# Kernel optimization log

Measured on AMD Instinct MI355X. Metric: run time of the kernel, lower is better.

Reference implementation:

```python
import jax, jax.numpy as jnp
import numpy as np

B, T, DIM = 4, 2048, 1024
H, DH = 16, 64  # num_heads, dim_head = dim // num_heads


def setup_inputs() -> dict:
    key = jax.random.key(0)
    k1, k2, k3 = jax.random.split(key, 3)
    x = jax.random.normal(k1, (B, T, DIM), dtype=jnp.float32)
    # nn.Linear weights stored as [out_features, in_features]
    w_qkv = jax.random.normal(k2, (3 * H * DH, DIM), dtype=jnp.float32) * (DIM ** -0.5)
    w_out = jax.random.normal(k3, (DIM, H * DH), dtype=jnp.float32) * ((H * DH) ** -0.5)
    b_out = jnp.zeros((DIM,), dtype=jnp.float32)
    return {"x": x, "w_qkv": w_qkv, "w_out": w_out, "b_out": b_out}


def reference(x, w_qkv, w_out, b_out):
    b, t, dim = x.shape
    # qkv projection (Linear, no bias): [b, t, 3*H*DH]
    qkv = jnp.einsum('btd,ed->bte', x, w_qkv)
    # einops 'b t (d k h) -> k b h t d' with k=3, h=H: dim_head outermost, heads innermost
    qkv = qkv.reshape(b, t, DH, 3, H)            # [b, t, d, k, h]
    qkv = jnp.transpose(qkv, (3, 0, 4, 1, 2))    # [k, b, h, t, d]
    q, k_, v = qkv[0], qkv[1], qkv[2]
    scale = dim ** -0.5  # note: scales by dim, not dim_head (faithful to source)
    attn = jnp.einsum('bhid,bhjd->bhij', q, k_) * scale
    attn = jax.nn.softmax(attn, axis=-1)
    out = jnp.einsum('bhij,bhjd->bhid', attn, v)  # [b, h, t, d]
    # 'b h t d -> b t (h d)'
    out = jnp.transpose(out, (0, 2, 1, 3)).reshape(b, t, H * DH)
    return jnp.einsum('bte,de->btd', out, w_out) + b_out
```

## Files before the change

### kernel.cpp

```cpp
#include <hip/hip_runtime.h>
#include <stdint.h>

typedef unsigned short ushort_t;
typedef __attribute__((ext_vector_type(8))) short short8;
typedef __attribute__((ext_vector_type(4))) short short4v;
typedef __attribute__((ext_vector_type(4))) float f32x4;
typedef __attribute__((ext_vector_type(16))) float f32x16;

#define B_ 4
#define T_ 2048
#define H_ 16
#define DH_ 64
#define DIM_ 1024
#define NE_ 3072
#define LOG2E 1.4426950408889634f

__device__ __forceinline__ ushort_t f2bf(float f) {
  union { float f; uint32_t u; } v; v.f = f;
  uint32_t u = v.u;
  uint32_t r = (u + 0x7FFFu + ((u >> 16) & 1u)) >> 16;
  return (ushort_t)r;
}
__device__ __forceinline__ void gload16(const void* g, void* l) {
  __builtin_amdgcn_global_load_lds(
      (__attribute__((address_space(1))) void*)g,
      (__attribute__((address_space(3))) void*)l, 16, 0, 0);
}
__device__ __forceinline__ uint32_t cvtpk(float a, float b) {
  uint32_t r;
  asm("v_cvt_pk_bf16_f32 %0, %1, %2" : "=v"(r) : "v"(a), "v"(b));
  return r;
}
__device__ __forceinline__ float exp2_asm(float x) {
  float r; asm("v_exp_f32 %0, %1" : "=v"(r) : "v"(x)); return r;
}

__global__ __launch_bounds__(256)
void cvt3(const float* __restrict__ a, ushort_t* __restrict__ oa, long nba,
          const float* __restrict__ b, ushort_t* __restrict__ ob, long nbb,
          const float* __restrict__ c, ushort_t* __restrict__ oc) {
  long i = ((long)blockIdx.x * 256 + threadIdx.x) * 4;
  const float* src; ushort_t* dst;
  if (i < nba)            { src = a; dst = oa; }
  else if (i < nba + nbb) { src = b; dst = ob; i -= nba; }
  else                    { src = c; dst = oc; i -= nba + nbb; }
  const float4 v = *(const float4*)(src + i);
  short4v o;
  o[0] = (short)f2bf(v.x); o[1] = (short)f2bf(v.y);
  o[2] = (short)f2bf(v.z); o[3] = (short)f2bf(v.w);
  *(short4v*)(dst + i) = o;
}

template<int MODE>
__global__ __launch_bounds__(256)
void gemm_bt(const ushort_t* __restrict__ A, const ushort_t* __restrict__ Bm,
             ushort_t* __restrict__ Cb, float* __restrict__ Cf,
             const float* __restrict__ bias, int M, int N, int K, int nb) {
  __shared__ __align__(16) ushort_t Alds[128 * 32];
  __shared__ __align__(16) ushort_t Blds[128 * 32];
  const int tid = threadIdx.x;
  const int wave = tid >> 6, lane = tid & 63;
  const int cpx = gridDim.x >> 3;
  const int bid = (blockIdx.x & 7) * cpx + (blockIdx.x >> 3);
  const int bm0 = (bid / nb) << 7, bn0 = (bid % nb) << 7;
  const int l4 = lane >> 4, l15 = lane & 15;
  const int srow = lane >> 2;
  const int scol = (lane & 3) * 8;
  const int wr = (wave >> 1) * 64, wc = (wave & 1) * 64;

  f32x4 acc[4][4];
#pragma unroll
  for (int i = 0; i < 4; ++i)
#pragma unroll
    for (int j = 0; j < 4; ++j) acc[i][j] = {0.f, 0.f, 0.f, 0.f};

  for (int k0 = 0; k0 < K; k0 += 32) {
    __syncthreads();
#pragma unroll
    for (int c = 0; c < 2; ++c) {
      const int r0 = wave * 32 + c * 16;
      gload16(A + (long)(bm0 + r0 + srow) * K + k0 + scol, Alds + r0 * 32);
      gload16(Bm + (long)(bn0 + r0 + srow) * K + k0 + scol, Blds + r0 * 32);
    }
    __syncthreads();
    short8 af[4], bfr[4];
#pragma unroll
    for (int i = 0; i < 4; ++i)
      af[i] = *(const short8*)(Alds + (wr + i * 16 + l15) * 32 + l4 * 8);
#pragma unroll
    for (int j = 0; j < 4; ++j)
      bfr[j] = *(const short8*)(Blds + (wc + j * 16 + l15) * 32 + l4 * 8);
#pragma unroll
    for (int i = 0; i < 4; ++i)
#pragma unroll
      for (int j = 0; j < 4; ++j)
        acc[i][j] = __builtin_amdgcn_mfma_f32_16x16x32_bf16(af[i], bfr[j], acc[i][j], 0, 0, 0);
  }

#pragma unroll
  for (int i = 0; i < 4; ++i) {
    const int row = bm0 + wr + i * 16 + l4 * 4;
#pragma unroll
    for (int j = 0; j < 4; ++j) {
      const int col = bn0 + wc + j * 16 + l15;
      if (MODE == 0) {
        const float mult = (((col >> 4) % 3) == 0) ? 0.04508422f : 1.f;
#pragma unroll
        for (int r = 0; r < 4; ++r)
          Cb[(long)(row + r) * N + col] = f2bf(acc[i][j][r] * mult);
      } else {
        const float add = bias[col];
#pragma unroll
        for (int r = 0; r < 4; ++r)
          Cf[(long)(row + r) * N + col] = acc[i][j][r] + add;
      }
    }
  }
}

__global__ __launch_bounds__(256)
void reorg(const ushort_t* __restrict__ qkv, ushort_t* __restrict__ Qh,
           ushort_t* __restrict__ Kh, ushort_t* __restrict__ Vth) {
  __shared__ __align__(16) ushort_t lds[8 * 3080];
  const int bid = blockIdx.x;
  const int tt = bid & 255, b = bid >> 8;
  const int t0 = tt * 8;
  const int tid = threadIdx.x;
  const short8* src = (const short8*)(qkv + ((long)(b * T_ + t0)) * NE_);
  short8* dst = (short8*)lds;
  for (int i = tid; i < 8 * 384; i += 256) {
    const int r = i / 384, c = i - r * 384;
    dst[r * 385 + c] = src[i];
  }
  __syncthreads();
  for (int i = tid; i < 16 * 8 * 8; i += 256) {
    const int dblk = i & 7, t = (i >> 3) & 7, h = i >> 6;
    short8 vq, vk;
#pragma unroll
    for (int e = 0; e < 8; ++e) {
      const int d = dblk * 8 + e;
      vq[e] = (short)lds[t * 3080 + d * 48 + h];
      vk[e] = (short)lds[t * 3080 + d * 48 + 16 + h];
    }
    const long o = ((long)((b * H_ + h) * T_) + t0 + t) * DH_ + dblk * 8;
    *(short8*)(Qh + o) = vq;
    *(short8*)(Kh + o) = vk;
  }
  for (int i = tid; i < 16 * 64; i += 256) {
    const int d = i & 63, h = i >> 6;
    short8 v0;
#pragma unroll
    for (int t = 0; t < 8; ++t) v0[t] = (short)lds[t * 3080 + d * 48 + 32 + h];
    const long o = ((long)((b * H_ + h) * DH_) + d) * T_ + t0;
    *(short8*)(Vth + o) = v0;
  }
}

#define MFMA32(a, b, c) __builtin_amdgcn_mfma_f32_32x32x16_bf16(a, b, c, 0, 0, 0)

__global__ __launch_bounds__(256, 4)
void attn_fwd6(const ushort_t* __restrict__ Qh, const ushort_t* __restrict__ Kh,
               const ushort_t* __restrict__ Vth, ushort_t* __restrict__ aout) {
  __shared__ __align__(16) ushort_t Kt[2][64 * 64];
  __shared__ __align__(16) ushort_t Vts[2][64 * 64];
  const int bid = blockIdx.x;
  const int xcd = bid & 7, idx = bid >> 3;
  const int bh = xcd + ((idx & 7) << 3);
  const int qb = idx >> 3;
  const int tid = threadIdx.x, wv = tid >> 6, lane = tid & 63;
  const int l31 = lane & 31, hi = lane >> 5, l7 = lane & 7, l8 = lane >> 3;
  const ushort_t* Qb = Qh + (long)bh * T_ * DH_;
  const ushort_t* Kb = Kh + (long)bh * T_ * DH_;
  const ushort_t* Vb = Vth + (long)bh * DH_ * T_;
  const int q = qb * 128 + wv * 32 + l31;

  short8 qf[4];
#pragma unroll
  for (int s = 0; s < 4; ++s)
    qf[s] = *(const short8*)(Qb + (long)q * DH_ + s * 16 + hi * 8);

  f32x16 acc0, acc1, z16;
#pragma unroll
  for (int i = 0; i < 16; ++i) { acc0[i] = 0.f; acc1[i] = 0.f; z16[i] = 0.f; }
  float lsum_part = 0.f;

  const int r0a = wv * 16;
  const int sl = ((l7 ^ l8) * 8);

#define STAGE(bufi, jj)                                                          \
  do {                                                                           \
    _Pragma("unroll")                                                            \
    for (int c = 0; c < 2; ++c) {                                                \
      const int rr = r0a + c * 8 + l8;                                           \
      gload16(Kb + (long)((jj) + rr) * DH_ + sl, &Kt[bufi][(r0a + c * 8) * 64]); \
      gload16(Vb + (long)rr * T_ + (jj) + sl, &Vts[bufi][(r0a + c * 8) * 64]);   \
    }                                                                            \
  } while (0)

  STAGE(0, 0);
  asm volatile("s_waitcnt vmcnt(0)" ::: "memory");
  __builtin_amdgcn_sched_barrier(0);
  __builtin_amdgcn_s_barrier();
  __builtin_amdgcn_sched_barrier(0);

  int buf = 0;
  for (int j0 = 0; j0 < T_; j0 += 64) {
    STAGE(buf ^ 1, (j0 + 64) & (T_ - 1));

    const ushort_t* Ktb = &Kt[buf][0];
    const ushort_t* Vtb = &Vts[buf][0];

    f32x16 sb0, sb1;
    __builtin_amdgcn_s_setprio(1);
#pragma unroll
    for (int s = 0; s < 4; ++s) {
      const int so = ((2 * s + hi) ^ l7) * 8;
      const short8 k0 = *(const short8*)(Ktb + (l31) * 64 + so);
      const short8 k1 = *(const short8*)(Ktb + (32 + l31) * 64 + so);
      sb0 = MFMA32(k0, qf[s], (s == 0) ? z16 : sb0);
      sb1 = MFMA32(k1, qf[s], (s == 0) ? z16 : sb1);
    }
    __builtin_amdgcn_s_setprio(0);

    float r0 = 0.f, r1 = 0.f, r2 = 0.f, r3 = 0.f;
#pragma unroll
    for (int i = 0; i < 16; i += 4) {
      sb0[i]     = exp2_asm(sb0[i]);     r0 += sb0[i];
      sb0[i + 1] = exp2_asm(sb0[i + 1]); r1 += sb0[i + 1];
      sb0[i + 2] = exp2_asm(sb0[i + 2]); r2 += sb0[i + 2];
      sb0[i + 3] = exp2_asm(sb0[i + 3]); r3 += sb0[i + 3];
    }
#pragma unroll
    for (int i = 0; i < 16; i += 4) {
      sb1[i]     = exp2_asm(sb1[i]);     r0 += sb1[i];
      sb1[i + 1] = exp2_asm(sb1[i + 1]); r1 += sb1[i + 1];
      sb1[i + 2] = exp2_asm(sb1[i + 2]); r2 += sb1[i + 2];
      sb1[i + 3] = exp2_asm(sb1[i + 3]); r3 += sb1[i + 3];
    }
    lsum_part += (r0 + r1) + (r2 + r3);

    short8 pf[4];
#pragma unroll
    for (int ks = 0; ks < 4; ++ks) {
      const f32x16& S = (ks < 2) ? sb0 : sb1;
      const int rb = (ks & 1) * 8;
      uint32_t wE0 = cvtpk(S[rb + 0], S[rb + 1]);
      uint32_t wE1 = cvtpk(S[rb + 2], S[rb + 3]);
      uint32_t wO0 = cvtpk(S[rb + 4], S[rb + 5]);
      uint32_t wO1 = cvtpk(S[rb + 6], S[rb + 7]);
      asm("v_permlane32_swap_b32 %0, %1" : "+v"(wE0), "+v"(wO0));
      asm("v_permlane32_swap_b32 %0, %1" : "+v"(wE1), "+v"(wO1));
      union { uint32_t u[4]; short8 v; } pk;
      pk.u[0] = wE0; pk.u[1] = wE1; pk.u[2] = wO0; pk.u[3] = wO1;
      pf[ks] = pk.v;
    }

    __builtin_amdgcn_s_setprio(1);
#pragma unroll
    for (int ks = 0; ks < 4; ++ks) {
      const int so = ((2 * ks + hi) ^ l7) * 8;
      const short8 v0 = *(const short8*)(Vtb + (l31) * 64 + so);
      const short8 v1 = *(const short8*)(Vtb + (32 + l31) * 64 + so);
      acc0 = MFMA32(v0, pf[ks], acc0);
      acc1 = MFMA32(v1, pf[ks], acc1);
    }
    __builtin_amdgcn_s_setprio(0);

    asm volatile("s_waitcnt vmcnt(0)" ::: "memory");
    __builtin_amdgcn_sched_barrier(0);
    __builtin_amdgcn_s_barrier();
    __builtin_amdgcn_sched_barrier(0);
    buf ^= 1;
  }

  const float lsum = lsum_part + __shfl_xor(lsum_part, 32);
  const float inv = 1.f / lsum;
  const int b = bh >> 4, h = bh & 15;
  ushort_t* orow = aout + ((long)(b * T_ + q)) * DIM_ + h * DH_;
#pragma unroll
  for (int vb = 0; vb < 2; ++vb)
#pragma unroll
    for (int rg = 0; rg < 4; ++rg) {
      short4v o4;
#pragma unroll
      for (int e = 0; e < 4; ++e) {
        const float val = ((vb == 0) ? acc0[rg * 4 + e] : acc1[rg * 4 + e]) * inv;
        o4[e] = (short)f2bf(val);
      }
      *(short4v*)(orow + vb * 32 + rg * 8 + hi * 4) = o4;
    }
}

extern "C" void kernel_launch(void* const* d_in, const int* in_sizes, int n_in,
                              void* d_out, int out_size, void* d_ws, size_t ws_size,
                              hipStream_t stream) {
  const float* x_f    = (const float*)d_in[0];
  const float* wqkv_f = (const float*)d_in[1];
  const float* wout_f = (const float*)d_in[2];
  const float* bout_f = (const float*)d_in[3];
  float* out = (float*)d_out;

  ushort_t* wqkv_bf = (ushort_t*)d_ws;
  ushort_t* wout_bf = wqkv_bf + (long)NE_ * DIM_;
  ushort_t* qkv     = wout_bf + (long)DIM_ * DIM_;
  ushort_t* R       = qkv + (long)B_ * T_ * NE_;
  ushort_t* x_bf = R;
  ushort_t* Qh   = R;
  ushort_t* Kh   = R + (long)B_ * H_ * T_ * DH_;
  ushort_t* Vth  = Kh + (long)B_ * H_ * T_ * DH_;
  ushort_t* aout = qkv;

  const long n_x = (long)B_ * T_ * DIM_;
  const long n_wq = (long)NE_ * DIM_;
  cvt3<<<dim3((int)((n_x + n_wq + (long)DIM_ * DIM_) / 1024)), dim3(256), 0, stream>>>(
      x_f, x_bf, n_x, wqkv_f, wqkv_bf, n_wq, wout_f, wout_bf);

  gemm_bt<0><<<dim3((8192 / 128) * (3072 / 128)), dim3(256), 0, stream>>>(
      x_bf, wqkv_bf, qkv, nullptr, nullptr, 8192, 3072, 1024, 3072 / 128);
  reorg<<<dim3(1024), dim3(256), 0, stream>>>(qkv, Qh, Kh, Vth);
  attn_fwd6<<<dim3(1024), dim3(256), 0, stream>>>(Qh, Kh, Vth, aout);
  gemm_bt<1><<<dim3((8192 / 128) * (1024 / 128)), dim3(256), 0, stream>>>(
      aout, wout_bf, nullptr, out, bout_f, 8192, 1024, 1024, 1024 / 128);
}
```

Before: 224.2 us.

## Replace GEMMs with 256x256 double-buffered, swizzled-LDS pipelined kernel

Both projection GEMMs now use 256x256 output tiles with 512 threads and a K-step of 64. LDS is double-buffered so the next tile's global loads are issued while MFMAs run on the current one. The LDS layout uses an XOR swizzle to avoid bank conflicts, and the wave schedule uses barrier phases and setprio. The aim is to raise operand reuse and hide load latency, but the grid shrinks a lot (384 and 128 blocks), which risks poor CU occupancy on the output projection.

```diff
diff --git a/kernel.cpp b/kernel.cpp
--- a/kernel.cpp
+++ b/kernel.cpp
@@ -51,71 +51,124 @@
   *(short4v*)(dst + i) = o;
 }
 
+#define MFMA16(a, b, c) __builtin_amdgcn_mfma_f32_16x16x32_bf16(a, b, c, 0, 0, 0)
+#define MFMA32(a, b, c) __builtin_amdgcn_mfma_f32_32x32x16_bf16(a, b, c, 0, 0, 0)
+
 template<int MODE>
-__global__ __launch_bounds__(256)
-void gemm_bt(const ushort_t* __restrict__ A, const ushort_t* __restrict__ Bm,
+__global__ __launch_bounds__(512, 2)
+void gemm256(const ushort_t* __restrict__ A, const ushort_t* __restrict__ Bm,
              ushort_t* __restrict__ Cb, float* __restrict__ Cf,
              const float* __restrict__ bias, int M, int N, int K, int nb) {
-  __shared__ __align__(16) ushort_t Alds[128 * 32];
-  __shared__ __align__(16) ushort_t Blds[128 * 32];
+  __shared__ __align__(16) ushort_t Al[2][256 * 64];
+  __shared__ __align__(16) ushort_t Bl[2][256 * 64];
   const int tid = threadIdx.x;
   const int wave = tid >> 6, lane = tid & 63;
   const int cpx = gridDim.x >> 3;
   const int bid = (blockIdx.x & 7) * cpx + (blockIdx.x >> 3);
-  const int bm0 = (bid / nb) << 7, bn0 = (bid % nb) << 7;
+  const int bm0 = (bid / nb) << 8, bn0 = (bid % nb) << 8;
   const int l4 = lane >> 4, l15 = lane & 15;
-  const int srow = lane >> 2;
-  const int scol = (lane & 3) * 8;
-  const int wr = (wave >> 1) * 64, wc = (wave & 1) * 64;
-
-  f32x4 acc[4][4];
-#pragma unroll
-  for (int i = 0; i < 4; ++i)
+  const int l7 = lane & 7, l8 = lane >> 3;
+  const int wm = wave >> 2, wn = wave & 3;
+  const int wrow0 = wm * 128, wcol0 = wn * 64;
+
+  const int sl = (l7 ^ l8) * 8;
+  const int r0a = wave * 32;
+
+#define GSTAGE(bufi, kk0)                                                          \
+  do {                                                                             \
+    _Pragma("unroll")                                                              \
+    for (int c = 0; c < 4; ++c) {                                                  \
+      const int rr = r0a + c * 8 + l8;                                             \
+      gload16(A + (long)(bm0 + rr) * K + (kk0) + sl, &Al[bufi][(r0a + c * 8) * 64]); \
+      gload16(Bm + (long)(bn0 + rr) * K + (kk0) + sl, &Bl[bufi][(r0a + c * 8) * 64]); \
+    }                                                                              \
+  } while (0)
+
+  f32x4 acc[8][4];
+#pragma unroll
+  for (int i = 0; i < 8; ++i)
 #pragma unroll
     for (int j = 0; j < 4; ++j) acc[i][j] = {0.f, 0.f, 0.f, 0.f};
 
-  for (int k0 = 0; k0 < K; k0 += 32) {
-    __syncthreads();
-#pragma unroll
-    for (int c = 0; c < 2; ++c) {
-      const int r0 = wave * 32 + c * 16;
-      gload16(A + (long)(bm0 + r0 + srow) * K + k0 + scol, Alds + r0 * 32);
-      gload16(Bm + (long)(bn0 + r0 + srow) * K + k0 + scol, Blds + r0 * 32);
-    }
-    __syncthreads();
-    short8 af[4], bfr[4];
-#pragma unroll
-    for (int i = 0; i < 4; ++i)
-      af[i] = *(const short8*)(Alds + (wr + i * 16 + l15) * 32 + l4 * 8);
-#pragma unroll
-    for (int j = 0; j < 4; ++j)
-      bfr[j] = *(const short8*)(Blds + (wc + j * 16 + l15) * 32 + l4 * 8);
-#pragma unroll
-    for (int i = 0; i < 4; ++i)
-#pragma unroll
-      for (int j = 0; j < 4; ++j)
-        acc[i][j] = __builtin_amdgcn_mfma_f32_16x16x32_bf16(af[i], bfr[j], acc[i][j], 0, 0, 0);
-  }
-
-#pragma unroll
-  for (int i = 0; i < 4; ++i) {
-    const int row = bm0 + wr + i * 16 + l4 * 4;
-#pragma unroll
-    for (int j = 0; j < 4; ++j) {
-      const int col = bn0 + wc + j * 16 + l15;
+  GSTAGE(0, 0);
+  asm volatile("s_waitcnt vmcnt(0)" ::: "memory");
+  __builtin_amdgcn_sched_barrier(0);
+  __builtin_amdgcn_s_barrier();
+  __builtin_amdgcn_sched_barrier(0);
+
+  const int NT = K >> 6;
+  int buf = 0;
+  for (int kt = 0; kt < NT; ++kt) {
+    const int k0 = kt << 6;
+    const ushort_t* Ab = &Al[buf][0];
+    const ushort_t* Bb = &Bl[buf][0];
+    short8 af[4][2];
+#pragma unroll
+    for (int p = 0; p < 4; ++p) {
+      const int mh = p >> 1, nh = p & 1;
+      if (nh == 0) {
+#pragma unroll
+        for (int fi = 0; fi < 4; ++fi) {
+          const int ar = wrow0 + mh * 64 + fi * 16 + l15;
+#pragma unroll
+          for (int kk = 0; kk < 2; ++kk)
+            af[fi][kk] = *(const short8*)(Ab + ar * 64 + ((4 * kk + l4) ^ l7) * 8);
+        }
+      }
+      short8 bf2[2][2];
+#pragma unroll
+      for (int fj = 0; fj < 2; ++fj) {
+        const int br = wcol0 + nh * 32 + fj * 16 + l15;
+#pragma unroll
+        for (int kk = 0; kk < 2; ++kk)
+          bf2[fj][kk] = *(const short8*)(Bb + br * 64 + ((4 * kk + l4) ^ l7) * 8);
+      }
+      if (p == 0 && kt < NT - 1) GSTAGE(buf ^ 1, k0 + 64);
+
+      __builtin_amdgcn_sched_barrier(0);
+      __builtin_amdgcn_s_barrier();
+      __builtin_amdgcn_sched_barrier(0);
+      __builtin_amdgcn_s_setprio(1);
+#pragma unroll
+      for (int fi = 0; fi < 4; ++fi)
+#pragma unroll
+        for (int fj = 0; fj < 2; ++fj)
+#pragma unroll
+          for (int kk = 0; kk < 2; ++kk)
+            acc[mh * 4 + fi][nh * 2 + fj] =
+                MFMA16(af[fi][kk], bf2[fj][kk], acc[mh * 4 + fi][nh * 2 + fj]);
+      __builtin_amdgcn_s_setprio(0);
+      __builtin_amdgcn_sched_barrier(0);
+      if (p == 3) {
+        asm volatile("s_waitcnt vmcnt(0)" ::: "memory");
+        __builtin_amdgcn_sched_barrier(0);
+      }
+      __builtin_amdgcn_s_barrier();
+      __builtin_amdgcn_sched_barrier(0);
+    }
+    buf ^= 1;
+  }
+
+#pragma unroll
+  for (int fi = 0; fi < 8; ++fi) {
+    const int row = bm0 + wrow0 + fi * 16 + l4 * 4;
+#pragma unroll
+    for (int fj = 0; fj < 4; ++fj) {
+      const int col = bn0 + wcol0 + fj * 16 + l15;
       if (MODE == 0) {
         const float mult = (((col >> 4) % 3) == 0) ? 0.04508422f : 1.f;
 #pragma unroll
         for (int r = 0; r < 4; ++r)
-          Cb[(long)(row + r) * N + col] = f2bf(acc[i][j][r] * mult);
+          Cb[(long)(row + r) * N + col] = f2bf(acc[fi][fj][r] * mult);
       } else {
         const float add = bias[col];
 #pragma unroll
         for (int r = 0; r < 4; ++r)
-          Cf[(long)(row + r) * N + col] = acc[i][j][r] + add;
-      }
-    }
-  }
+          Cf[(long)(row + r) * N + col] = acc[fi][fj][r] + add;
+      }
+    }
+  }
+#undef GSTAGE
 }
 
 __global__ __launch_bounds__(256)
@@ -155,8 +208,6 @@
     *(short8*)(Vth + o) = v0;
   }
 }
-
-#define MFMA32(a, b, c) __builtin_amdgcn_mfma_f32_32x32x16_bf16(a, b, c, 0, 0, 0)
 
 __global__ __launch_bounds__(256, 4)
 void attn_fwd6(const ushort_t* __restrict__ Qh, const ushort_t* __restrict__ Kh,
@@ -289,6 +340,7 @@
       }
       *(short4v*)(orow + vb * 32 + rg * 8 + hi * 4) = o4;
     }
+#undef STAGE
 }
 
 extern "C" void kernel_launch(void* const* d_in, const int* in_sizes, int n_in,
@@ -315,10 +367,10 @@
   cvt3<<<dim3((int)((n_x + n_wq + (long)DIM_ * DIM_) / 1024)), dim3(256), 0, stream>>>(
       x_f, x_bf, n_x, wqkv_f, wqkv_bf, n_wq, wout_f, wout_bf);
 
-  gemm_bt<0><<<dim3((8192 / 128) * (3072 / 128)), dim3(256), 0, stream>>>(
-      x_bf, wqkv_bf, qkv, nullptr, nullptr, 8192, 3072, 1024, 3072 / 128);
+  gemm256<0><<<dim3((8192 / 256) * (3072 / 256)), dim3(512), 0, stream>>>(
+      x_bf, wqkv_bf, qkv, nullptr, nullptr, 8192, 3072, 1024, 3072 / 256);
   reorg<<<dim3(1024), dim3(256), 0, stream>>>(qkv, Qh, Kh, Vth);
   attn_fwd6<<<dim3(1024), dim3(256), 0, stream>>>(Qh, Kh, Vth, aout);
-  gemm_bt<1><<<dim3((8192 / 128) * (1024 / 128)), dim3(256), 0, stream>>>(
-      aout, wout_bf, nullptr, out, bout_f, 8192, 1024, 1024, 1024 / 128);
-}
+  gemm256<1><<<dim3((8192 / 256) * (1024 / 256)), dim3(512), 0, stream>>>(
+      aout, wout_bf, nullptr, out, bout_f, 8192, 1024, 1024, 1024 / 256);
+}
```

Measured after the change: 237.7 us. +6.0%, slower.
